# Optimization experiments

Hardware: AMD Instinct MI355X
Metric: run time of the kernel (lower is better)

The kernel has to match this reference:

```python
import jax, jax.numpy as jnp
import numpy as np

N_ATOMS = 8192
MAX_NEIGHBORS = 12
MAX_RADIUS = 8.0
NUM_BINS = 50
WIDTH = 0.2


def setup_inputs() -> dict:
    key = jax.random.key(0)
    # uniform distances in [0,1): all within max_radius, so every node has
    # >= MAX_NEIGHBORS valid neighbors -> fixed output shape N*MAX_NEIGHBORS
    dm = jax.random.uniform(key, (N_ATOMS, N_ATOMS), dtype=jnp.float32)
    return {"distance_matrix": dm}


def reference(distance_matrix):
    n = distance_matrix.shape[0]
    # radius threshold: entries beyond max_radius are excluded from selection
    masked = jnp.where(distance_matrix <= MAX_RADius_const(), distance_matrix, jnp.inf) if False else jnp.where(distance_matrix <= MAX_RADIUS, distance_matrix, jnp.inf)
    # per-node smallest-k neighbors == original global-sort + per-node first-k
    _, nbr_idx = jax.lax.top_k(-masked, MAX_NEIGHBORS)  # [n, k]
    dists = jnp.take_along_axis(distance_matrix, nbr_idx, axis=1)  # [n, k]
    src = jnp.broadcast_to(jnp.arange(n, dtype=nbr_idx.dtype)[:, None], (n, MAX_NEIGHBORS))
    edge_index = jnp.stack([src, nbr_idx], axis=-1).reshape(-1, 2)  # [n*k, 2]
    # Gaussian RBF expansion
    centers = jnp.linspace(0.0, 1.0, NUM_BINS)  # [NUM_BINS]
    z = (dists[..., None] - centers) / WIDTH  # [n, k, NUM_BINS]
    edge_features = jnp.exp(-0.5 * z * z).reshape(-1, NUM_BINS)  # [n*k, NUM_BINS]
    return edge_index, edge_features
```

## Files before the change

kernel.cpp:

```cpp
#include <hip/hip_runtime.h>
#include <math.h>


#define N_ATOMS 8192
#define K 12
#define NBINS 50
#define CAP 192
#define WAVES 4
#define BLOCK (WAVES * 64)
#define MAX_RADIUS 8.0f
#define CAND_T 0.01f

typedef float f4 __attribute__((ext_vector_type(4)));

__global__ __launch_bounds__(BLOCK, 8) void edge_kernel(const float* __restrict__ dm,
                                                        float* __restrict__ out) {
    const int wave = threadIdx.x >> 6;
    const int lane = threadIdx.x & 63;
    const int row = blockIdx.x * WAVES + wave;
    const float* rowp = dm + (size_t)row * N_ATOMS;
    const f4* row4 = (const f4*)rowp;

    __shared__ unsigned long long s_keys[WAVES][CAP];
    __shared__ int s_cnt[WAVES];
    __shared__ int s_selidx[WAVES][K];
    __shared__ float s_seldist[WAVES][K];

    if (lane == 0) s_cnt[wave] = 0;

    #pragma unroll
    for (int i = 0; i < 8; ++i) {
        f4 v[4];
        #pragma unroll
        for (int j = 0; j < 4; ++j)
            v[j] = row4[lane + (i * 4 + j) * 64];
        #pragma unroll
        for (int j = 0; j < 4; ++j) {
            int bidx = (lane + (i * 4 + j) * 64) * 4;
            #pragma unroll
            for (int c = 0; c < 4; ++c) {
                float d = v[j][c];
                if (d < CAND_T) {
                    int pos = atomicAdd(&s_cnt[wave], 1);
                    if (pos < CAP)
                        s_keys[wave][pos] =
                            ((unsigned long long)__float_as_uint(d) << 32) |
                            (unsigned int)(bidx + c);
                }
            }
        }
    }
    __syncthreads();

    const int total = s_cnt[wave];

    if (total >= K && total <= CAP) {
        for (int j = lane; j < total; j += 64) {
            unsigned long long kj = s_keys[wave][j];
            int rank = 0;
            for (int m2 = 0; m2 < total; ++m2)
                rank += (s_keys[wave][m2] < kj) ? 1 : 0;
            if (rank < K) {
                s_selidx[wave][rank] = (int)(kj & 0xFFFFFFFFull);
                s_seldist[wave][rank] =
                    __uint_as_float((unsigned int)(kj >> 32));
            }
        }
    } else {
        unsigned long long last = 0ull;
        for (int r = 0; r < K; ++r) {
            unsigned long long best = ~0ull;
            for (int i = 0; i < 32; ++i) {
                int v4 = lane + i * 64;
                f4 v = row4[v4];
                int bidx = v4 * 4;
                #pragma unroll
                for (int c = 0; c < 4; ++c) {
                    float d = v[c];
                    float md = (d <= MAX_RADIUS) ? d
                                                 : __uint_as_float(0x7F800000u);
                    unsigned long long key =
                        ((unsigned long long)__float_as_uint(md) << 32) |
                        (unsigned int)(bidx + c);
                    if (((r == 0) || (key > last)) && key < best) best = key;
                }
            }
            #pragma unroll
            for (int off = 32; off > 0; off >>= 1) {
                unsigned long long other = __shfl_xor(best, off, 64);
                if (other < best) best = other;
            }
            if (lane == 0) {
                int idx = (int)(best & 0xFFFFFFFFull);
                s_selidx[wave][r] = idx;
                s_seldist[wave][r] = rowp[idx];
            }
            last = best;
        }
    }

    float* out_ei = out;
    float* out_ef = out + (size_t)N_ATOMS * K * 2;
    if (lane < 2 * K) {
        int r = lane >> 1, comp = lane & 1;
        __builtin_nontemporal_store(
            comp ? (float)s_selidx[wave][r] : (float)row,
            &out_ei[((size_t)row * K + r) * 2 + comp]);
    }
    for (int t = lane; t < K * NBINS; t += 64) {
        int r = t / NBINS, b = t - r * NBINS;
        float d = s_seldist[wave][r];
        float z = (d - (float)b * (1.0f / 49.0f)) * 5.0f;
        __builtin_nontemporal_store(__expf(-0.5f * z * z),
                                    &out_ef[(size_t)row * K * NBINS + t]);
    }
}

extern "C" void kernel_launch(void* const* d_in, const int* in_sizes, int n_in,
                              void* d_out, int out_size, void* d_ws, size_t ws_size,
                              hipStream_t stream) {
    const float* dm = (const float*)d_in[0];
    float* out = (float*)d_out;
    edge_kernel<<<N_ATOMS / WAVES, BLOCK, 0, stream>>>(dm, out);
}
```

Baseline: 365.2 us.

## Assign one 512-thread block per row instead of one wave per row

Each row is now handled by a full 512-thread block instead of a single wave. Every thread issues all four of its vector loads up front, using nontemporal loads, before filtering candidates with shared atomics. This gives more memory-level parallelism per row and shorter per-thread loops, aimed at the bandwidth-bound 256MB read. The cost is block-wide syncs, more blocks to launch, and contention on a single shared atomic counter per block. The fallback path now runs on only one wave while the others sit idle.

```diff
diff --git a/kernel.cpp b/kernel.cpp
--- a/kernel.cpp
+++ b/kernel.cpp
@@ -6,8 +6,7 @@
 #define K 12
 #define NBINS 50
 #define CAP 192
-#define WAVES 4
-#define BLOCK (WAVES * 64)
+#define BLOCK 512
 #define MAX_RADIUS 8.0f
 #define CAND_T 0.01f
 
@@ -15,68 +14,67 @@
 
 __global__ __launch_bounds__(BLOCK, 8) void edge_kernel(const float* __restrict__ dm,
                                                         float* __restrict__ out) {
-    const int wave = threadIdx.x >> 6;
-    const int lane = threadIdx.x & 63;
-    const int row = blockIdx.x * WAVES + wave;
+    const int tid = threadIdx.x;
+    const int row = blockIdx.x;
     const float* rowp = dm + (size_t)row * N_ATOMS;
     const f4* row4 = (const f4*)rowp;
 
-    __shared__ unsigned long long s_keys[WAVES][CAP];
-    __shared__ int s_cnt[WAVES];
-    __shared__ int s_selidx[WAVES][K];
-    __shared__ float s_seldist[WAVES][K];
+    __shared__ unsigned long long s_keys[CAP];
+    __shared__ int s_cnt;
+    __shared__ int s_selidx[K];
+    __shared__ float s_seldist[K];
 
-    if (lane == 0) s_cnt[wave] = 0;
+    f4 v[4];
+    #pragma unroll
+    for (int i = 0; i < 4; ++i)
+        v[i] = __builtin_nontemporal_load(&row4[tid + i * BLOCK]);
+
+    if (tid == 0) s_cnt = 0;
+    __syncthreads();
 
     #pragma unroll
-    for (int i = 0; i < 8; ++i) {
-        f4 v[4];
+    for (int i = 0; i < 4; ++i) {
+        int bidx = (tid + i * BLOCK) * 4;
         #pragma unroll
-        for (int j = 0; j < 4; ++j)
-            v[j] = row4[lane + (i * 4 + j) * 64];
-        #pragma unroll
-        for (int j = 0; j < 4; ++j) {
-            int bidx = (lane + (i * 4 + j) * 64) * 4;
-            #pragma unroll
-            for (int c = 0; c < 4; ++c) {
-                float d = v[j][c];
-                if (d < CAND_T) {
-                    int pos = atomicAdd(&s_cnt[wave], 1);
-                    if (pos < CAP)
-                        s_keys[wave][pos] =
-                            ((unsigned long long)__float_as_uint(d) << 32) |
-                            (unsigned int)(bidx + c);
-                }
+        for (int c = 0; c < 4; ++c) {
+            float d = v[i][c];
+            if (d < CAND_T) {
+                int pos = atomicAdd(&s_cnt, 1);
+                if (pos < CAP)
+                    s_keys[pos] =
+                        ((unsigned long long)__float_as_uint(d) << 32) |
+                        (unsigned int)(bidx + c);
             }
         }
     }
     __syncthreads();
 
-    const int total = s_cnt[wave];
+    const int total = s_cnt;
 
     if (total >= K && total <= CAP) {
-        for (int j = lane; j < total; j += 64) {
-            unsigned long long kj = s_keys[wave][j];
+        for (int j = tid; j < total; j += BLOCK) {
+            unsigned long long kj = s_keys[j];
             int rank = 0;
             for (int m2 = 0; m2 < total; ++m2)
-                rank += (s_keys[wave][m2] < kj) ? 1 : 0;
+                rank += (s_keys[m2] < kj) ? 1 : 0;
             if (rank < K) {
-                s_selidx[wave][rank] = (int)(kj & 0xFFFFFFFFull);
-                s_seldist[wave][rank] =
+                s_selidx[rank] = (int)(kj & 0xFFFFFFFFull);
+                s_seldist[rank] =
                     __uint_as_float((unsigned int)(kj >> 32));
             }
         }
-    } else {
+    } else if (tid < 64) {
+        const int lane = tid;
         unsigned long long last = 0ull;
         for (int r = 0; r < K; ++r) {
             unsigned long long best = ~0ull;
             for (int i = 0; i < 32; ++i) {
-                int v4 = lane + i * 64;
-                f4 v = row4[v4];
-                int bidx = v4 * 4;
+                int v4i = lane + i * 64;
+                f4 w = __builtin_nontemporal_load(&row4[v4i]);
+                int bidx = v4i * 4;
                 #pragma unroll
                 for (int c = 0; c < 4; ++c) {
-                    float d = v[c];
+                    float d = w[c];
                     float md = (d <= MAX_RADIUS) ? d
                                                  : __uint_as_float(0x7F800000u);
                     unsigned long long key =
@@ -92,24 +90,25 @@
             }
             if (lane == 0) {
                 int idx = (int)(best & 0xFFFFFFFFull);
-                s_selidx[wave][r] = idx;
-                s_seldist[wave][r] = rowp[idx];
+                s_selidx[r] = idx;
+                s_seldist[r] = rowp[idx];
             }
             last = best;
         }
     }
+    __syncthreads();
 
     float* out_ei = out;
     float* out_ef = out + (size_t)N_ATOMS * K * 2;
-    if (lane < 2 * K) {
-        int r = lane >> 1, comp = lane & 1;
+    if (tid < 2 * K) {
+        int r = tid >> 1, comp = tid & 1;
         __builtin_nontemporal_store(
-            comp ? (float)s_selidx[wave][r] : (float)row,
+            comp ? (float)s_selidx[r] : (float)row,
             &out_ei[((size_t)row * K + r) * 2 + comp]);
     }
-    for (int t = lane; t < K * NBINS; t += 64) {
+    for (int t = tid; t < K * NBINS; t += BLOCK) {
         int r = t / NBINS, b = t - r * NBINS;
-        float d = s_seldist[wave][r];
+        float d = s_seldist[r];
         float z = (d - (float)b * (1.0f / 49.0f)) * 5.0f;
         __builtin_nontemporal_store(__expf(-0.5f * z * z),
                                     &out_ef[(size_t)row * K * NBINS + t]);
@@ -121,5 +120,5 @@
                               hipStream_t stream) {
     const float* dm = (const float*)d_in[0];
     float* out = (float*)d_out;
-    edge_kernel<<<N_ATOMS / WAVES, BLOCK, 0, stream>>>(dm, out);
+    edge_kernel<<<N_ATOMS, BLOCK, 0, stream>>>(dm, out);
 }
```

New measurement: 340.2 us, median of 2. 6.9% less time.
